# Kernel optimization log

Measured on AMD Instinct MI355X. Metric: run time of the kernel, lower is better.

Reference implementation:

```python
import jax, jax.numpy as jnp
import numpy as np
from jax import lax

N, OC, IC, K = 32, 256, 256, 3
H = W = 56
STRIDE = 1
PADDING = 1
SPARSITY = 0.9  # fraction of zero weights


def setup_inputs() -> dict:
    key = jax.random.key(0)
    k_in, k_w, k_b, k_m = jax.random.split(key, 4)
    input = jax.random.normal(k_in, (N, IC, H, W), dtype=jnp.float32)
    weight = jax.random.normal(k_w, (OC, IC, K, K), dtype=jnp.float32) * 0.05
    bias = jax.random.normal(k_b, (OC,), dtype=jnp.float32) * 0.05
    mask = jax.random.bernoulli(k_m, p=1.0 - SPARSITY, shape=(OC, IC, K, K))
    return {"input": input, "weight": weight, "bias": bias, "mask": mask}


def reference(input, weight, bias, mask):
    # SparseConv2d stores only nonzero weights (W_val at W_idx); mathematically this
    # is a dense conv2d with the masked weight tensor.
    w = jnp.where(mask, weight, jnp.zeros((), dtype=weight.dtype))
    out = lax.conv_general_dilated(
        input, w,
        window_strides=(STRIDE, STRIDE),
        padding=[(PADDING, PADDING), (PADDING, PADDING)],
        dimension_numbers=("NCHW", "OIHW", "NCHW"),
    )
    return out + bias[None, :, None, None]
```

## Files before the change

kernel.cpp:

```cpp
#include <hip/hip_runtime.h>

constexpr int NB=32, ICC=256, OCC=256, HH=56, WW=56;
constexpr int HW=HH*WW, CHW=ICC*HW;
constexpr int YT=14, MT=2;
constexpr int LROW=58;
constexpr int PAD=36;
constexpr int LDS_ELEMS=6*LROW*PAD;

using short8  = __attribute__((ext_vector_type(8))) short;
using short4v = __attribute__((ext_vector_type(4))) short;
using f32x4   = __attribute__((ext_vector_type(4))) float;

__device__ inline unsigned bf16rne(float x){
  unsigned u = __float_as_uint(x);
  return (u + 0x7fffu + ((u>>16)&1u)) >> 16;
}

__global__ __launch_bounds__(256) void pack_weights(
    const float* __restrict__ w, const int* __restrict__ mask,
    unsigned short* __restrict__ wb){
  const int oc = blockIdx.x, ic = threadIdx.x;
  const int base = (oc*ICC + ic)*9;
  #pragma unroll
  for (int j=0;j<9;++j){
    float v = (mask[base+j] != 0) ? w[base+j] : 0.f;
    wb[(j*OCC + oc)*ICC + ic] = (unsigned short)bf16rne(v);
  }
}

__global__ __launch_bounds__(256,2) void conv_mfma(
    const float* __restrict__ in, const unsigned short* __restrict__ wb,
    const float* __restrict__ bias, float* __restrict__ out){
  __shared__ unsigned short xt[LDS_ELEMS];

  const int lid  = blockIdx.x;
  const int xcd  = lid & 7, slot = lid >> 3;
  const int ngrp = slot / 28, rem = slot - ngrp*28;
  const int mt   = rem / 14,  yt  = rem - mt*14;
  const int n    = xcd + 8*ngrp;
  const int y0   = yt*4, ocb = mt*128;

  const int tid  = threadIdx.x;
  const int lane = tid & 63, wv = tid >> 6;
  const int q    = lane >> 4, l16 = lane & 15;

  for (int i = tid; i < LDS_ELEMS/2; i += 256) ((unsigned*)xt)[i] = 0u;

  const int ocw = ocb + (wv & 1)*64;
  const int pxw = (wv >> 1)*112;

  int pbase[7];
  #pragma unroll
  for (int p=0;p<7;++p){
    int px = pxw + p*16 + l16;
    int yl = px / 56, x = px - yl*56;
    pbase[p] = (yl*LROW + x)*(PAD*2) + q*16;
  }

  f32x4 acc[4][7];
  #pragma unroll
  for (int s=0;s<4;++s)
    #pragma unroll
    for (int p=0;p<7;++p) acc[s][p] = (f32x4){0.f,0.f,0.f,0.f};

  const int rskipA = (yt==0)      ? 0 : -1;
  const int rskipB = (yt==YT-1)   ? 5 : -1;

  __syncthreads();

  for (int ch=0; ch<8; ++ch){
    const int ic0 = ch*32;

    #pragma unroll
    for (int i=0;i<6;++i){
      int idx = tid + i*256;
      if (idx < 1344){
        int r  = idx / 224;
        int r2 = idx - r*224;
        int xg = r2 >> 4, icp = r2 & 15;
        if (r != rskipA && r != rskipB){
          int y = y0 - 1 + r;
          const float* gp = in + n*CHW + (ic0 + icp*2)*HW + y*WW + xg*4;
          float4 g0 = *(const float4*)gp;
          float4 g1 = *(const float4*)(gp + HW);
          unsigned w0 = bf16rne(g0.x) | (bf16rne(g1.x)<<16);
          unsigned w1 = bf16rne(g0.y) | (bf16rne(g1.y)<<16);
          unsigned w2 = bf16rne(g0.z) | (bf16rne(g1.z)<<16);
          unsigned w3 = bf16rne(g0.w) | (bf16rne(g1.w)<<16);
          unsigned* dp = (unsigned*)xt + (r*LROW + 1 + xg*4)*(PAD/2) + icp;
          dp[0]         = w0;
          dp[PAD/2]     = w1;
          dp[PAD]       = w2;
          dp[3*(PAD/2)] = w3;
        }
      }
    }
    __syncthreads();

    #pragma unroll
    for (int kh=0;kh<3;++kh){
      #pragma unroll
      for (int kw=0;kw<3;++kw){
        const int j = kh*3 + kw;
        const unsigned short* wp = wb + (j*OCC + ocw + l16)*ICC + ic0 + q*8;
        short8 a0 = *(const short8*)(wp          );
        short8 a1 = *(const short8*)(wp + 16*ICC );
        short8 a2 = *(const short8*)(wp + 32*ICC );
        short8 a3 = *(const short8*)(wp + 48*ICC );
        const int doff = (kh*LROW + kw)*(PAD*2);
        #pragma unroll
        for (int p=0;p<7;++p){
          const char* bp = (const char*)xt + pbase[p] + doff;
          short4v blo = *(const short4v*)(bp    );
          short4v bhi = *(const short4v*)(bp + 8);
          short8 b = __builtin_shufflevector(blo, bhi, 0,1,2,3,4,5,6,7);
          acc[0][p] = __builtin_amdgcn_mfma_f32_16x16x32_bf16(a0, b, acc[0][p], 0,0,0);
          acc[1][p] = __builtin_amdgcn_mfma_f32_16x16x32_bf16(a1, b, acc[1][p], 0,0,0);
          acc[2][p] = __builtin_amdgcn_mfma_f32_16x16x32_bf16(a2, b, acc[2][p], 0,0,0);
          acc[3][p] = __builtin_amdgcn_mfma_f32_16x16x32_bf16(a3, b, acc[3][p], 0,0,0);
        }
      }
    }
    __syncthreads();
  }

  #pragma unroll
  for (int s=0;s<4;++s){
    const int oc4 = ocw + s*16 + q*4;
    float4 bv = *(const float4*)(bias + oc4);
    #pragma unroll
    for (int i=0;i<4;++i){
      const float bb = (i==0)?bv.x:(i==1)?bv.y:(i==2)?bv.z:bv.w;
      float* op = out + (n*OCC + oc4 + i)*HW + y0*WW + pxw + l16;
      #pragma unroll
      for (int p=0;p<7;++p){
        op[p*16] = acc[s][p][i] + bb;
      }
    }
  }
}

extern "C" void kernel_launch(void* const* d_in, const int* in_sizes, int n_in,
                              void* d_out, int out_size, void* d_ws, size_t ws_size,
                              hipStream_t stream) {
  const float* in   = (const float*)d_in[0];
  const float* w    = (const float*)d_in[1];
  const float* bias = (const float*)d_in[2];
  const int*   mask = (const int*)d_in[3];
  float*       out  = (float*)d_out;
  unsigned short* wb = (unsigned short*)d_ws;

  pack_weights<<<OCC, 256, 0, stream>>>(w, mask, wb);
  conv_mfma<<<8*4*MT*YT, 256, 0, stream>>>(in, wb, bias, out);
}
```

Baseline: 368.6 us.

## Double-buffer LDS input tiles and prefetch next channel chunk into registers

Splits the input staging into a global load into registers and a later LDS write, and doubles the LDS tile buffer. The loads for the next 32-channel chunk are issued before the MFMA compute on the current chunk, and the bf16 packing and LDS write happen afterwards into the other buffer. This also drops one barrier per chunk. The aim is to hide global memory latency behind the MFMA work, at the cost of 48 extra VGPRs for the prefetched float4s and twice the LDS, which may reduce occupancy below the two blocks per CU the launch bounds request.

```diff
diff --git a/kernel.cpp b/kernel.cpp
--- a/kernel.cpp
+++ b/kernel.cpp
@@ -6,6 +6,7 @@
 constexpr int LROW=58;
 constexpr int PAD=36;
 constexpr int LDS_ELEMS=6*LROW*PAD;
+constexpr int BUF_BYTES=LDS_ELEMS*2;
 
 using short8  = __attribute__((ext_vector_type(8))) short;
 using short4v = __attribute__((ext_vector_type(4))) short;
@@ -31,7 +32,7 @@
 __global__ __launch_bounds__(256,2) void conv_mfma(
     const float* __restrict__ in, const unsigned short* __restrict__ wb,
     const float* __restrict__ bias, float* __restrict__ out){
-  __shared__ unsigned short xt[LDS_ELEMS];
+  __shared__ unsigned short xt[2*LDS_ELEMS];
 
   const int lid  = blockIdx.x;
   const int xcd  = lid & 7, slot = lid >> 3;
@@ -44,7 +45,7 @@
   const int lane = tid & 63, wv = tid >> 6;
   const int q    = lane >> 4, l16 = lane & 15;
 
-  for (int i = tid; i < LDS_ELEMS/2; i += 256) ((unsigned*)xt)[i] = 0u;
+  for (int i = tid; i < LDS_ELEMS; i += 256) ((unsigned*)xt)[i] = 0u;
 
   const int ocw = ocb + (wv & 1)*64;
   const int pxw = (wv >> 1)*112;
@@ -66,11 +67,10 @@
   const int rskipA = (yt==0)      ? 0 : -1;
   const int rskipB = (yt==YT-1)   ? 5 : -1;
 
-  __syncthreads();
+  float4 g0v[6], g1v[6];
 
-  for (int ch=0; ch<8; ++ch){
+  auto stage_load = [&](int ch){
     const int ic0 = ch*32;
-
     #pragma unroll
     for (int i=0;i<6;++i){
       int idx = tid + i*256;
@@ -81,13 +81,29 @@
         if (r != rskipA && r != rskipB){
           int y = y0 - 1 + r;
           const float* gp = in + n*CHW + (ic0 + icp*2)*HW + y*WW + xg*4;
-          float4 g0 = *(const float4*)gp;
-          float4 g1 = *(const float4*)(gp + HW);
+          g0v[i] = *(const float4*)gp;
+          g1v[i] = *(const float4*)(gp + HW);
+        }
+      }
+    }
+  };
+
+  auto stage_write = [&](int buf){
+    unsigned* base = (unsigned*)xt + buf*(LDS_ELEMS/2);
+    #pragma unroll
+    for (int i=0;i<6;++i){
+      int idx = tid + i*256;
+      if (idx < 1344){
+        int r  = idx / 224;
+        int r2 = idx - r*224;
+        int xg = r2 >> 4, icp = r2 & 15;
+        if (r != rskipA && r != rskipB){
+          float4 g0 = g0v[i], g1 = g1v[i];
           unsigned w0 = bf16rne(g0.x) | (bf16rne(g1.x)<<16);
           unsigned w1 = bf16rne(g0.y) | (bf16rne(g1.y)<<16);
           unsigned w2 = bf16rne(g0.z) | (bf16rne(g1.z)<<16);
           unsigned w3 = bf16rne(g0.w) | (bf16rne(g1.w)<<16);
-          unsigned* dp = (unsigned*)xt + (r*LROW + 1 + xg*4)*(PAD/2) + icp;
+          unsigned* dp = base + (r*LROW + 1 + xg*4)*(PAD/2) + icp;
           dp[0]         = w0;
           dp[PAD/2]     = w1;
           dp[PAD]       = w2;
@@ -95,8 +111,11 @@
         }
       }
     }
-    __syncthreads();
+  };
 
+  auto compute = [&](int buf, int ch){
+    const int ic0 = ch*32;
+    const char* xb = (const char*)xt + buf*BUF_BYTES;
     #pragma unroll
     for (int kh=0;kh<3;++kh){
       #pragma unroll
@@ -110,7 +129,7 @@
         const int doff = (kh*LROW + kw)*(PAD*2);
         #pragma unroll
         for (int p=0;p<7;++p){
-          const char* bp = (const char*)xt + pbase[p] + doff;
+          const char* bp = xb + pbase[p] + doff;
           short4v blo = *(const short4v*)(bp    );
           short4v bhi = *(const short4v*)(bp + 8);
           short8 b = __builtin_shufflevector(blo, bhi, 0,1,2,3,4,5,6,7);
@@ -121,7 +140,21 @@
         }
       }
     }
+  };
+
+  stage_load(0);
+  __syncthreads();
+  stage_write(0);
+  __syncthreads();
+
+  int cur = 0;
+  #pragma unroll 2
+  for (int ch=0; ch<8; ++ch){
+    if (ch < 7) stage_load(ch+1);
+    compute(cur, ch);
+    if (ch < 7) stage_write(cur^1);
     __syncthreads();
+    cur ^= 1;
   }
 
   #pragma unroll
```

Result: slower. 422.8 us (+14.7%).

## Pre-pack input to NHWC bf16 and double-buffer LDS via direct global-to-LDS loads

Applied to the files above, without the earlier changes.

A new kernel converts the fp32 NCHW input to a bf16 channels-last layout in workspace. The conv kernel then streams each 32-channel chunk straight into double-buffered LDS with global_load_lds, using an XOR swizzle against bank conflicts, so the next chunk loads while the current one computes. Padding is handled by pointing out-of-bounds lanes at a shared zero slot instead of zero-filling LDS. The cost is an extra launch plus a full read and write of the input, and the old fp32 path stays as a fallback when the workspace is too small.

```diff
diff --git a/kernel.cpp b/kernel.cpp
--- a/kernel.cpp
+++ b/kernel.cpp
@@ -3,6 +3,8 @@
 constexpr int NB=32, ICC=256, OCC=256, HH=56, WW=56;
 constexpr int HW=HH*WW, CHW=ICC*HW;
 constexpr int YT=14, MT=2;
+constexpr int BUFB = 6*56*64;
+constexpr int ZOFF = 2*BUFB;
 constexpr int LROW=58;
 constexpr int PAD=36;
 constexpr int LDS_ELEMS=6*LROW*PAD;
@@ -28,10 +30,38 @@
   }
 }
 
+__global__ __launch_bounds__(256) void pack_input(
+    const float* __restrict__ in, unsigned short* __restrict__ inb){
+  __shared__ unsigned short t[56*258];
+  const int bid = blockIdx.x;
+  const int n = bid/56, y = bid - n*56;
+  const float* src = in + (size_t)n*CHW + y*WW;
+  const int tid = threadIdx.x;
+  #pragma unroll
+  for (int i=0;i<14;++i){
+    int idx = tid + i*256;
+    int ic = idx / 14, xg = idx - ic*14;
+    float4 v = *(const float4*)(src + ic*HW + xg*4);
+    int xb = xg*4;
+    t[(xb+0)*258 + ic] = (unsigned short)bf16rne(v.x);
+    t[(xb+1)*258 + ic] = (unsigned short)bf16rne(v.y);
+    t[(xb+2)*258 + ic] = (unsigned short)bf16rne(v.z);
+    t[(xb+3)*258 + ic] = (unsigned short)bf16rne(v.w);
+  }
+  __syncthreads();
+  unsigned* dst = (unsigned*)(inb + (size_t)(n*56+y)*56*256);
+  #pragma unroll
+  for (int i=0;i<28;++i){
+    int idx = tid + i*256;
+    int x = idx >> 7, icp = idx & 127;
+    dst[idx] = *(const unsigned*)&t[x*258 + icp*2];
+  }
+}
+
 __global__ __launch_bounds__(256,2) void conv_mfma(
-    const float* __restrict__ in, const unsigned short* __restrict__ wb,
+    const unsigned short* __restrict__ inb, const unsigned short* __restrict__ wb,
     const float* __restrict__ bias, float* __restrict__ out){
-  __shared__ unsigned short xt[LDS_ELEMS];
+  __shared__ unsigned short xt[(2*BUFB + 16)/2];
 
   const int lid  = blockIdx.x;
   const int xcd  = lid & 7, slot = lid >> 3;
@@ -44,17 +74,130 @@
   const int lane = tid & 63, wv = tid >> 6;
   const int q    = lane >> 4, l16 = lane & 15;
 
-  for (int i = tid; i < LDS_ELEMS/2; i += 256) ((unsigned*)xt)[i] = 0u;
-
   const int ocw = ocb + (wv & 1)*64;
   const int pxw = (wv >> 1)*112;
 
-  int pbase[7];
+  int xp[7], yl[7];
   #pragma unroll
   for (int p=0;p<7;++p){
     int px = pxw + p*16 + l16;
-    int yl = px / 56, x = px - yl*56;
-    pbase[p] = (yl*LROW + x)*(PAD*2) + q*16;
+    yl[p] = px / 56;  xp[p] = px - yl[p]*56;
+  }
+
+  f32x4 acc[4][7];
+  #pragma unroll
+  for (int s=0;s<4;++s)
+    #pragma unroll
+    for (int p=0;p<7;++p) acc[s][p] = (f32x4){0.f,0.f,0.f,0.f};
+
+  if (tid == 0) *(f32x4*)((char*)xt + ZOFF) = (f32x4){0.f,0.f,0.f,0.f};
+
+  const unsigned short* nb = inb + (size_t)n*(56*56*256);
+
+  auto stage = [&](int buf, int ch){
+    const int ic0 = ch*32;
+    #pragma unroll
+    for (int i=0;i<6;++i){
+      int idx = tid + i*256;
+      if (idx < 1344){
+        int r   = idx / 224;
+        int rm  = idx - r*224;
+        int cc  = rm >> 2, sub = rm & 3;
+        int y   = y0 - 1 + r;
+        y = y < 0 ? 0 : (y > 55 ? 55 : y);
+        int icg = sub ^ ((cc>>1)&3);
+        const unsigned short* gp = nb + (y*56 + cc)*256 + ic0 + icg*8;
+        char* lp = (char*)xt + buf*BUFB + idx*16;
+        __builtin_amdgcn_global_load_lds(
+            (const __attribute__((address_space(1))) void*)gp,
+            (__attribute__((address_space(3))) void*)lp, 16, 0, 0);
+      }
+    }
+  };
+
+  auto compute = [&](int buf, int ch){
+    const int ic0 = ch*32;
+    const char* xb = (const char*)xt + buf*BUFB;
+    const char* zp = (const char*)xt + ZOFF;
+    #pragma unroll
+    for (int kh=0;kh<3;++kh){
+      #pragma unroll
+      for (int kw=0;kw<3;++kw){
+        const int j = kh*3 + kw;
+        const unsigned short* wp = wb + (j*OCC + ocw + l16)*ICC + ic0 + q*8;
+        short8 a0 = *(const short8*)(wp          );
+        short8 a1 = *(const short8*)(wp + 16*ICC );
+        short8 a2 = *(const short8*)(wp + 32*ICC );
+        short8 a3 = *(const short8*)(wp + 48*ICC );
+        #pragma unroll
+        for (int p=0;p<7;++p){
+          int xq = xp[p] + kw - 1;
+          int yq = y0 - 1 + yl[p] + kh;
+          bool valid = ((unsigned)xq < 56u) & ((unsigned)yq < 56u);
+          int addr = (((yl[p]+kh)*56 + xq)<<6) + ((q ^ ((xq>>1)&3))<<4);
+          const char* bp = valid ? (xb + addr) : zp;
+          short8 b = *(const short8*)bp;
+          acc[0][p] = __builtin_amdgcn_mfma_f32_16x16x32_bf16(a0, b, acc[0][p], 0,0,0);
+          acc[1][p] = __builtin_amdgcn_mfma_f32_16x16x32_bf16(a1, b, acc[1][p], 0,0,0);
+          acc[2][p] = __builtin_amdgcn_mfma_f32_16x16x32_bf16(a2, b, acc[2][p], 0,0,0);
+          acc[3][p] = __builtin_amdgcn_mfma_f32_16x16x32_bf16(a3, b, acc[3][p], 0,0,0);
+        }
+      }
+    }
+  };
+
+  stage(0, 0);
+  __syncthreads();
+
+  for (int ch=0; ch<8; ++ch){
+    if (ch < 7) stage((ch+1)&1, ch+1);
+    compute(ch&1, ch);
+    __syncthreads();
+  }
+
+  #pragma unroll
+  for (int s=0;s<4;++s){
+    const int oc4 = ocw + s*16 + q*4;
+    float4 bv = *(const float4*)(bias + oc4);
+    #pragma unroll
+    for (int i=0;i<4;++i){
+      const float bb = (i==0)?bv.x:(i==1)?bv.y:(i==2)?bv.z:bv.w;
+      float* op = out + (n*OCC + oc4 + i)*HW + y0*WW + pxw + l16;
+      #pragma unroll
+      for (int p=0;p<7;++p){
+        op[p*16] = acc[s][p][i] + bb;
+      }
+    }
+  }
+}
+
+__global__ __launch_bounds__(256,2) void conv_mfma_f32(
+    const float* __restrict__ in, const unsigned short* __restrict__ wb,
+    const float* __restrict__ bias, float* __restrict__ out){
+  __shared__ unsigned short xt[LDS_ELEMS];
+
+  const int lid  = blockIdx.x;
+  const int xcd  = lid & 7, slot = lid >> 3;
+  const int ngrp = slot / 28, rem = slot - ngrp*28;
+  const int mt   = rem / 14,  yt  = rem - mt*14;
+  const int n    = xcd + 8*ngrp;
+  const int y0   = yt*4, ocb = mt*128;
+
+  const int tid  = threadIdx.x;
+  const int lane = tid & 63, wv = tid >> 6;
+  const int q    = lane >> 4, l16 = lane & 15;
+
+  for (int i = tid; i < LDS_ELEMS/2; i += 256) ((unsigned*)xt)[i] = 0u;
+
+  const int ocw = ocb + (wv & 1)*64;
+  const int pxw = (wv >> 1)*112;
+
+  int pbase[7];
+  #pragma unroll
+  for (int p=0;p<7;++p){
+    int px = pxw + p*16 + l16;
+    int ylv = px / 56, x = px - ylv*56;
+    pbase[p] = (ylv*LROW + x)*(PAD*2) + q*16;
   }
 
   f32x4 acc[4][7];
@@ -70,7 +213,6 @@
 
   for (int ch=0; ch<8; ++ch){
     const int ic0 = ch*32;
-
     #pragma unroll
     for (int i=0;i<6;++i){
       int idx = tid + i*256;
@@ -150,6 +292,15 @@
   float*       out  = (float*)d_out;
   unsigned short* wb = (unsigned short*)d_ws;
 
+  const size_t WB_BYTES  = (size_t)9*OCC*ICC*2;
+  const size_t INB_BYTES = (size_t)NB*HH*WW*ICC*2;
+
   pack_weights<<<OCC, 256, 0, stream>>>(w, mask, wb);
-  conv_mfma<<<8*4*MT*YT, 256, 0, stream>>>(in, wb, bias, out);
-}
+  if (ws_size >= WB_BYTES + INB_BYTES){
+    unsigned short* inb = (unsigned short*)((char*)d_ws + WB_BYTES);
+    pack_input<<<NB*HH, 256, 0, stream>>>(in, inb);
+    conv_mfma<<<8*4*MT*YT, 256, 0, stream>>>(inb, wb, bias, out);
+  } else {
+    conv_mfma_f32<<<8*4*MT*YT, 256, 0, stream>>>(in, wb, bias, out);
+  }
+}
```

Measured after the change: 345.8 us. 1.07x faster.
